# Kernel tuning notes

Hardware: AMD Instinct MI355X
Metric: run time of the kernel (lower is better)

The kernel has to match this reference:

```python
import jax, jax.numpy as jnp
import numpy as np

ALPHA = 0.5  # leak/integration rate of the EI cell

B, L, D = 512, 64, 784
N_EXC, N_INH, N_CLS = 128, 32, 10


def setup_inputs() -> dict:
    key = jax.random.key(0)
    ks = jax.random.split(key, 11)
    s_in = 1.0 / np.sqrt(D)
    s_e = 1.0 / np.sqrt(N_EXC)
    s_i = 1.0 / np.sqrt(N_INH)
    return {
        "x_seq": jax.random.normal(ks[0], (B, L, D), jnp.float32),
        "Wxe": jax.random.normal(ks[1], (N_EXC, D), jnp.float32) * s_in,
        "Wxi": jax.random.normal(ks[2], (N_INH, D), jnp.float32) * s_in,
        "Wee": jax.random.normal(ks[3], (N_EXC, N_EXC), jnp.float32) * s_e,
        "Wie": jax.random.normal(ks[4], (N_EXC, N_INH), jnp.float32) * s_i,
        "Wei": jax.random.normal(ks[5], (N_INH, N_EXC), jnp.float32) * s_e,
        "Wii": jax.random.normal(ks[6], (N_INH, N_INH), jnp.float32) * s_i,
        "be": jax.random.normal(ks[7], (N_EXC,), jnp.float32) * 0.01,
        "bi": jax.random.normal(ks[8], (N_INH,), jnp.float32) * 0.01,
        "W_ro": jax.random.normal(ks[9], (N_CLS, N_EXC), jnp.float32) * s_e,
        "b_ro": jax.random.normal(ks[10], (N_CLS,), jnp.float32) * 0.01,
    }


def reference(x_seq, Wxe, Wxi, Wee, Wie, Wei, Wii, be, bi, W_ro, b_ro):
    # Dale's law: rectify weight magnitudes so exc/inh signs are structural.
    Wxe_p, Wxi_p = jax.nn.relu(Wxe), jax.nn.relu(Wxi)
    Wee_p, Wie_p = jax.nn.relu(Wee), jax.nn.relu(Wie)
    Wei_p, Wii_p = jax.nn.relu(Wei), jax.nn.relu(Wii)

    def step(carry, x_t):  # x_t: [B, D]
        e, i = carry
        r_e = jax.nn.relu(e)
        r_i = jax.nn.relu(i)
        exc_e = x_t @ Wxe_p.T + r_e @ Wee_p.T          # [B, n_exc]
        inh_e = r_i @ Wie_p.T                           # [B, n_exc]
        exc_i = x_t @ Wxi_p.T + r_e @ Wei_p.T           # [B, n_inh]
        inh_i = r_i @ Wii_p.T                           # [B, n_inh]
        e_new = (1.0 - ALPHA) * e + ALPHA * (exc_e - inh_e + be)
        i_new = (1.0 - ALPHA) * i + ALPHA * (exc_i - inh_i + bi)
        r_e_new = jax.nn.relu(e_new)
        r_i_new = jax.nn.relu(i_new)
        bal_e = exc_e - inh_e
        bal_i = exc_i - inh_i
        logits_t = r_e_new @ W_ro.T + b_ro              # readout(F.relu(e))
        return (e_new, i_new), (logits_t, r_e_new, r_i_new, bal_e, bal_i)

    Bn = x_seq.shape[0]
    e0 = jnp.zeros((Bn, Wee.shape[0]), x_seq.dtype)
    i0 = jnp.zeros((Bn, Wii.shape[0]), x_seq.dtype)
    _, outs = jax.lax.scan(step, (e0, i0), jnp.swapaxes(x_seq, 0, 1))  # time-major
    logits_seq, r_e_seq, r_i_seq, bal_e_seq, bal_i_seq = (
        jnp.swapaxes(o, 0, 1) for o in outs)  # back to [B, L, ...]
    return logits_seq, logits_seq[:, -1, :], r_e_seq, r_i_seq, bal_e_seq, bal_i_seq
```

## Files before the change

### kernel.cpp

```cpp
#include <hip/hip_runtime.h>

#define NE 128
#define NI 32
#define NT 160
#define NC 10
#define BB 512
#define LL 64
#define DD 784
#define KP 800
#define MM (BB*LL)

#define G_OFF   0
#define G_SZ    (NT*NT)
#define WH_OFF  (G_OFF + G_SZ)
#define WL_OFF  (WH_OFF + 64000)
#define U_OFF   (WL_OFF + 64000)
#define U_SZ    (MM*NT)

#define O_LOGITS 0
#define O_LAST   327680
#define O_RE     332800
#define O_RI     4527104
#define O_BALE   5575680
#define O_BALI   9769984

#define LDS_BARRIER() asm volatile("s_waitcnt lgkmcnt(0)\n\ts_barrier" ::: "memory")

typedef __attribute__((ext_vector_type(8))) short short8;
typedef __attribute__((ext_vector_type(4))) float af4;

static __device__ __forceinline__ unsigned short f2bf(float f) {
  unsigned u = __float_as_uint(f);
  return (unsigned short)((u + 0x7FFFu + ((u >> 16) & 1u)) >> 16);
}
static __device__ __forceinline__ float bf2f(unsigned short h) {
  return __uint_as_float((unsigned)h << 16);
}

__global__ void prep_kernel(const float* __restrict__ Wxe, const float* __restrict__ Wxi,
                            const float* __restrict__ Wee, const float* __restrict__ Wie,
                            const float* __restrict__ Wei, const float* __restrict__ Wii,
                            float* __restrict__ ws) {
  int idx = blockIdx.x * blockDim.x + threadIdx.x;
  const int total = G_SZ + NT * KP;
  if (idx >= total) return;
  if (idx < G_SZ) {
    int k = idx / NT, j = idx % NT;
    float g;
    if (j < NE) {
      if (k < NE) g =  fmaxf(Wee[j*NE + k], 0.f);
      else        g = -fmaxf(Wie[j*NI + (k-NE)], 0.f);
    } else {
      int ji = j - NE;
      if (k < NE) g =  fmaxf(Wei[ji*NE + k], 0.f);
      else        g = -fmaxf(Wii[ji*NI + (k-NE)], 0.f);
    }
    ws[G_OFF + k*NT + j] = g;
  } else {
    int t = idx - G_SZ;
    int n = t / KP, k = t - n * KP;
    float v = 0.f;
    if (k < DD)
      v = (n < NE) ? fmaxf(Wxe[n*DD + k], 0.f) : fmaxf(Wxi[(n-NE)*DD + k], 0.f);
    unsigned short h = f2bf(v);
    unsigned short l = f2bf(v - bf2f(h));
    ((unsigned short*)(ws + WH_OFF))[t] = h;
    ((unsigned short*)(ws + WL_OFF))[t] = l;
  }
}

__global__ __launch_bounds__(256, 1) void gemm_kernel(const float* __restrict__ X,
                                                      const float* __restrict__ ws,
                                                      float* __restrict__ U) {
  const int tid  = threadIdx.x;
  const int lane = tid & 63;
  const int wave = tid >> 6;
  const int n16  = lane & 15;
  const int quad = lane >> 4;
  const int mbase = blockIdx.x * 128 + wave * 32;

  const unsigned short* Wh = (const unsigned short*)(ws + WH_OFF);
  const unsigned short* Wl = (const unsigned short*)(ws + WL_OFF);

  af4 acc[2][10];
  #pragma unroll
  for (int ms = 0; ms < 2; ++ms)
    #pragma unroll
    for (int nt = 0; nt < 10; ++nt)
      #pragma unroll
      for (int r = 0; r < 4; ++r) acc[ms][nt][r] = 0.f;

  const float* xrow[2] = { X + (size_t)(mbase + n16) * DD,
                           X + (size_t)(mbase + 16 + n16) * DD };

  for (int ks = 0; ks < 24; ++ks) {
    const int kb = ks * 32 + quad * 8;
    short8 ah[2], al[2];
    #pragma unroll
    for (int ms = 0; ms < 2; ++ms) {
      float4 v0 = *(const float4*)(xrow[ms] + kb);
      float4 v1 = *(const float4*)(xrow[ms] + kb + 4);
      float f[8] = {v0.x, v0.y, v0.z, v0.w, v1.x, v1.y, v1.z, v1.w};
      #pragma unroll
      for (int j = 0; j < 8; ++j) {
        unsigned short h = f2bf(f[j]);
        ah[ms][j] = (short)h;
        al[ms][j] = (short)f2bf(f[j] - bf2f(h));
      }
    }
    short8 bh[10], bl[10];
    #pragma unroll
    for (int nt = 0; nt < 10; ++nt) {
      const size_t off = (size_t)(nt * 16 + n16) * KP + kb;
      bh[nt] = *(const short8*)(Wh + off);
      bl[nt] = *(const short8*)(Wl + off);
    }
    #pragma unroll
    for (int ms = 0; ms < 2; ++ms)
      #pragma unroll
      for (int nt = 0; nt < 10; ++nt) {
        acc[ms][nt] = __builtin_amdgcn_mfma_f32_16x16x32_bf16(ah[ms], bh[nt], acc[ms][nt], 0, 0, 0);
        acc[ms][nt] = __builtin_amdgcn_mfma_f32_16x16x32_bf16(ah[ms], bl[nt], acc[ms][nt], 0, 0, 0);
        acc[ms][nt] = __builtin_amdgcn_mfma_f32_16x16x32_bf16(al[ms], bh[nt], acc[ms][nt], 0, 0, 0);
      }
  }

  {
    const int kb = 768 + quad * 8;
    const bool ok = kb < DD;
    short8 ah[2], al[2];
    #pragma unroll
    for (int ms = 0; ms < 2; ++ms) {
      float f[8] = {0,0,0,0,0,0,0,0};
      if (ok) {
        float4 v0 = *(const float4*)(xrow[ms] + kb);
        float4 v1 = *(const float4*)(xrow[ms] + kb + 4);
        f[0]=v0.x; f[1]=v0.y; f[2]=v0.z; f[3]=v0.w;
        f[4]=v1.x; f[5]=v1.y; f[6]=v1.z; f[7]=v1.w;
      }
      #pragma unroll
      for (int j = 0; j < 8; ++j) {
        unsigned short h = f2bf(f[j]);
        ah[ms][j] = (short)h;
        al[ms][j] = (short)f2bf(f[j] - bf2f(h));
      }
    }
    short8 bh[10], bl[10];
    #pragma unroll
    for (int nt = 0; nt < 10; ++nt) {
      const size_t off = (size_t)(nt * 16 + n16) * KP + kb;
      bh[nt] = *(const short8*)(Wh + off);
      bl[nt] = *(const short8*)(Wl + off);
    }
    #pragma unroll
    for (int ms = 0; ms < 2; ++ms)
      #pragma unroll
      for (int nt = 0; nt < 10; ++nt) {
        acc[ms][nt] = __builtin_amdgcn_mfma_f32_16x16x32_bf16(ah[ms], bh[nt], acc[ms][nt], 0, 0, 0);
        acc[ms][nt] = __builtin_amdgcn_mfma_f32_16x16x32_bf16(ah[ms], bl[nt], acc[ms][nt], 0, 0, 0);
        acc[ms][nt] = __builtin_amdgcn_mfma_f32_16x16x32_bf16(al[ms], bh[nt], acc[ms][nt], 0, 0, 0);
      }
  }

  #pragma unroll
  for (int ms = 0; ms < 2; ++ms)
    #pragma unroll
    for (int nt = 0; nt < 10; ++nt)
      #pragma unroll
      for (int r = 0; r < 4; ++r) {
        const int row = mbase + ms * 16 + quad * 4 + r;
        U[(size_t)row * NT + nt * 16 + n16] = acc[ms][nt][r];
      }
}

__global__ __launch_bounds__(256, 2) void recur_kernel(
    const float* __restrict__ ws,
    const float* __restrict__ be, const float* __restrict__ bi,
    float* __restrict__ out) {
  __shared__ float rbuf[2][NT];
  __shared__ float balbuf[2][NT];
  __shared__ float biasL[NT];

  const int tid  = threadIdx.x;
  const int lane = tid & 63;
  const int wave = tid >> 6;
  const int jc   = (wave << 3) | (lane & 7);
  const int kc   = (lane >> 3) & 7;
  const int j0   = jc * 5;
  const int k0   = kc * 20;
  const int b    = blockIdx.x;

  const float* G = ws + G_OFF;
  const float* U = ws + U_OFF;

  float g[20][5];
  #pragma unroll
  for (int kk = 0; kk < 20; ++kk)
    #pragma unroll
    for (int c = 0; c < 5; ++c)
      g[kk][c] = G[(size_t)(k0 + kk) * NT + j0 + c];

  if (tid < NT) biasL[tid] = (tid < NE) ? be[tid] : bi[tid - NE];
  for (int i = tid; i < 2 * NT; i += 256) (&rbuf[0][0])[i] = 0.f;

  const bool owner = (kc == 0);
  float u[5];
  if (owner) {
    const size_t ub = ((size_t)b * LL) * NT + j0;
    #pragma unroll
    for (int c = 0; c < 5; ++c) u[c] = U[ub + c];
  }
  float s[5];
  #pragma unroll
  for (int c = 0; c < 5; ++c) s[c] = 0.f;

  __syncthreads();

  for (int l = 0; l < LL; ++l) {
    const int p = l & 1;
    if (l > 0) {
      const size_t ob = (size_t)b * LL + (l - 1);
      if (tid < NE) {
        out[O_RE   + ob * NE + tid] = rbuf[p][tid];
        out[O_BALE + ob * NE + tid] = balbuf[p][tid];
      } else if (tid < NT) {
        const int j2 = tid - NE;
        out[O_RI   + ob * NI + j2] = rbuf[p][NE + j2];
        out[O_BALI + ob * NI + j2] = balbuf[p][NE + j2];
      }
    }
    float nu[5];
    if (owner && l + 1 < LL) {
      const size_t nb = ((size_t)b * LL + (l + 1)) * NT + j0;
      #pragma unroll
      for (int c = 0; c < 5; ++c) nu[c] = U[nb + c];
    }
    float a[5];
    #pragma unroll
    for (int c = 0; c < 5; ++c) a[c] = 0.f;
    #pragma unroll
    for (int kk4 = 0; kk4 < 5; ++kk4) {
      float4 rv = *(const float4*)(&rbuf[p][k0 + kk4 * 4]);
      #pragma unroll
      for (int c = 0; c < 5; ++c)
        a[c] += rv.x * g[kk4*4+0][c] + rv.y * g[kk4*4+1][c]
              + rv.z * g[kk4*4+2][c] + rv.w * g[kk4*4+3][c];
    }
    #pragma unroll
    for (int c = 0; c < 5; ++c) {
      float v = a[c];
      v += __shfl_xor(v, 8, 64);
      v += __shfl_xor(v, 16, 64);
      v += __shfl_xor(v, 32, 64);
      a[c] = v;
    }
    if (owner) {
      #pragma unroll
      for (int c = 0; c < 5; ++c) {
        float bal = a[c] + u[c];
        balbuf[1 - p][j0 + c] = bal;
        float sn = 0.5f * (s[c] + bal + biasL[j0 + c]);
        s[c] = sn;
        rbuf[1 - p][j0 + c] = fmaxf(sn, 0.f);
      }
      #pragma unroll
      for (int c = 0; c < 5; ++c) u[c] = nu[c];
    }
    LDS_BARRIER();
  }
  {
    const size_t ob = (size_t)b * LL + 63;
    if (tid < NE) {
      out[O_RE   + ob * NE + tid] = rbuf[0][tid];
      out[O_BALE + ob * NE + tid] = balbuf[0][tid];
    } else if (tid < NT) {
      const int j2 = tid - NE;
      out[O_RI   + ob * NI + j2] = rbuf[0][NE + j2];
      out[O_BALI + ob * NI + j2] = balbuf[0][NE + j2];
    }
  }
}

__global__ __launch_bounds__(256) void logits_kernel(const float* __restrict__ Wro,
                                                     const float* __restrict__ bro,
                                                     float* __restrict__ out) {
  __shared__ float WroL[NC * 132];
  __shared__ float broL[NC];
  const int tid = threadIdx.x;
  for (int i = tid; i < NC * NE; i += 256) {
    int c = i >> 7, k = i & 127;
    WroL[c * 132 + k] = Wro[i];
  }
  if (tid < NC) broL[tid] = bro[tid];
  __syncthreads();
  const int idx = blockIdx.x * 256 + tid;
  const int m = idx / 10, c = idx - m * 10;
  const float* re = out + O_RE + (size_t)m * NE;
  float v = broL[c];
  #pragma unroll
  for (int t4 = 0; t4 < 32; ++t4) {
    float4 rv = *(const float4*)(re + t4 * 4);
    float4 wv = *(const float4*)(&WroL[c * 132 + t4 * 4]);
    v += rv.x * wv.x + rv.y * wv.y + rv.z * wv.z + rv.w * wv.w;
  }
  out[O_LOGITS + (size_t)m * NC + c] = v;
  if ((m & 63) == 63) out[O_LAST + (size_t)(m >> 6) * NC + c] = v;
}

extern "C" void kernel_launch(void* const* d_in, const int* in_sizes, int n_in,
                              void* d_out, int out_size, void* d_ws, size_t ws_size,
                              hipStream_t stream) {
  const float* x   = (const float*)d_in[0];
  const float* Wxe = (const float*)d_in[1];
  const float* Wxi = (const float*)d_in[2];
  const float* Wee = (const float*)d_in[3];
  const float* Wie = (const float*)d_in[4];
  const float* Wei = (const float*)d_in[5];
  const float* Wii = (const float*)d_in[6];
  const float* be  = (const float*)d_in[7];
  const float* bi  = (const float*)d_in[8];
  const float* Wro = (const float*)d_in[9];
  const float* bro = (const float*)d_in[10];
  float* ws  = (float*)d_ws;
  float* out = (float*)d_out;

  hipLaunchKernelGGL(prep_kernel, dim3((G_SZ + NT*KP + 255)/256), dim3(256), 0, stream,
                     Wxe, Wxi, Wee, Wie, Wei, Wii, ws);
  hipLaunchKernelGGL(gemm_kernel, dim3(MM/128), dim3(256), 0, stream,
                     x, ws, ws + U_OFF);
  hipLaunchKernelGGL(recur_kernel, dim3(BB), dim3(256), 0, stream,
                     ws, be, bi, out);
  hipLaunchKernelGGL(logits_kernel, dim3(MM * NC / 256), dim3(256), 0, stream,
                     Wro, bro, out);
}
```

Baseline: 314.3 us.

## Shrink GEMM tile per wave, prefetch X, use packed bf16 split conversion

```diff
diff --git a/kernel.cpp b/kernel.cpp
--- a/kernel.cpp
+++ b/kernel.cpp
@@ -35,6 +35,22 @@
 }
 static __device__ __forceinline__ float bf2f(unsigned short h) {
   return __uint_as_float((unsigned)h << 16);
+}
+
+static __device__ __forceinline__ void cvt_split8(const float* f, short8& ah, short8& al) {
+  union { short8 s; unsigned u[4]; } H, L;
+  #pragma unroll
+  for (int p = 0; p < 4; ++p) {
+    float lo = f[2*p], hi = f[2*p+1];
+    unsigned h;
+    asm("v_cvt_pk_bf16_f32 %0, %1, %2" : "=v"(h) : "v"(lo), "v"(hi));
+    float rl = lo - __uint_as_float(h << 16);
+    float rh = hi - __uint_as_float(h & 0xffff0000u);
+    unsigned l;
+    asm("v_cvt_pk_bf16_f32 %0, %1, %2" : "=v"(l) : "v"(rl), "v"(rh));
+    H.u[p] = h; L.u[p] = l;
+  }
+  ah = H.s; al = L.s;
 }
 
 __global__ void prep_kernel(const float* __restrict__ Wxe, const float* __restrict__ Wxi,
@@ -69,7 +85,7 @@
   }
 }
 
-__global__ __launch_bounds__(256, 1) void gemm_kernel(const float* __restrict__ X,
+__global__ __launch_bounds__(256, 2) void gemm_kernel(const float* __restrict__ X,
                                                       const float* __restrict__ ws,
                                                       float* __restrict__ U) {
   const int tid  = threadIdx.x;
@@ -77,35 +93,38 @@
   const int wave = tid >> 6;
   const int n16  = lane & 15;
   const int quad = lane >> 4;
-  const int mbase = blockIdx.x * 128 + wave * 32;
+  const int mbase = blockIdx.x * 64 + wave * 16;
 
   const unsigned short* Wh = (const unsigned short*)(ws + WH_OFF);
   const unsigned short* Wl = (const unsigned short*)(ws + WL_OFF);
 
-  af4 acc[2][10];
-  #pragma unroll
-  for (int ms = 0; ms < 2; ++ms)
-    #pragma unroll
-    for (int nt = 0; nt < 10; ++nt)
-      #pragma unroll
-      for (int r = 0; r < 4; ++r) acc[ms][nt][r] = 0.f;
-
-  const float* xrow[2] = { X + (size_t)(mbase + n16) * DD,
-                           X + (size_t)(mbase + 16 + n16) * DD };
+  af4 acc[10];
+  #pragma unroll
+  for (int nt = 0; nt < 10; ++nt)
+    #pragma unroll
+    for (int r = 0; r < 4; ++r) acc[nt][r] = 0.f;
+
+  const float* xrow = X + (size_t)(mbase + n16) * DD;
+
+  float fa[8];
+  {
+    const int kb = quad * 8;
+    float4 v0 = *(const float4*)(xrow + kb);
+    float4 v1 = *(const float4*)(xrow + kb + 4);
+    fa[0]=v0.x; fa[1]=v0.y; fa[2]=v0.z; fa[3]=v0.w;
+    fa[4]=v1.x; fa[5]=v1.y; fa[6]=v1.z; fa[7]=v1.w;
+  }
 
   for (int ks = 0; ks < 24; ++ks) {
     const int kb = ks * 32 + quad * 8;
-    short8 ah[2], al[2];
-    #pragma unroll
-    for (int ms = 0; ms < 2; ++ms) {
-      float4 v0 = *(const float4*)(xrow[ms] + kb);
-      float4 v1 = *(const float4*)(xrow[ms] + kb + 4);
-      float f[8] = {v0.x, v0.y, v0.z, v0.w, v1.x, v1.y, v1.z, v1.w};
-      #pragma unroll
-      for (int j = 0; j < 8; ++j) {
-        unsigned short h = f2bf(f[j]);
-        ah[ms][j] = (short)h;
-        al[ms][j] = (short)f2bf(f[j] - bf2f(h));
+    float nf[8] = {0,0,0,0,0,0,0,0};
+    {
+      const int nkb = kb + 32;
+      if (nkb < DD) {
+        float4 v0 = *(const float4*)(xrow + nkb);
+        float4 v1 = *(const float4*)(xrow + nkb + 4);
+        nf[0]=v0.x; nf[1]=v0.y; nf[2]=v0.z; nf[3]=v0.w;
+        nf[4]=v1.x; nf[5]=v1.y; nf[6]=v1.z; nf[7]=v1.w;
       }
     }
     short8 bh[10], bl[10];
@@ -115,36 +134,20 @@
       bh[nt] = *(const short8*)(Wh + off);
       bl[nt] = *(const short8*)(Wl + off);
     }
-    #pragma unroll
-    for (int ms = 0; ms < 2; ++ms)
-      #pragma unroll
-      for (int nt = 0; nt < 10; ++nt) {
-        acc[ms][nt] = __builtin_amdgcn_mfma_f32_16x16x32_bf16(ah[ms], bh[nt], acc[ms][nt], 0, 0, 0);
-        acc[ms][nt] = __builtin_amdgcn_mfma_f32_16x16x32_bf16(ah[ms], bl[nt], acc[ms][nt], 0, 0, 0);
-        acc[ms][nt] = __builtin_amdgcn_mfma_f32_16x16x32_bf16(al[ms], bh[nt], acc[ms][nt], 0, 0, 0);
-      }
+    short8 ah, al;
+    cvt_split8(fa, ah, al);
+    #pragma unroll
+    for (int nt = 0; nt < 10; ++nt) {
+      acc[nt] = __builtin_amdgcn_mfma_f32_16x16x32_bf16(ah, bh[nt], acc[nt], 0, 0, 0);
+      acc[nt] = __builtin_amdgcn_mfma_f32_16x16x32_bf16(ah, bl[nt], acc[nt], 0, 0, 0);
+      acc[nt] = __builtin_amdgcn_mfma_f32_16x16x32_bf16(al, bh[nt], acc[nt], 0, 0, 0);
+    }
+    #pragma unroll
+    for (int j = 0; j < 8; ++j) fa[j] = nf[j];
   }
 
   {
     const int kb = 768 + quad * 8;
-    const bool ok = kb < DD;
-    short8 ah[2], al[2];
-    #pragma unroll
-    for (int ms = 0; ms < 2; ++ms) {
-      float f[8] = {0,0,0,0,0,0,0,0};
-      if (ok) {
-        float4 v0 = *(const float4*)(xrow[ms] + kb);
-        float4 v1 = *(const float4*)(xrow[ms] + kb + 4);
-        f[0]=v0.x; f[1]=v0.y; f[2]=v0.z; f[3]=v0.w;
-        f[4]=v1.x; f[5]=v1.y; f[6]=v1.z; f[7]=v1.w;
-      }
-      #pragma unroll
-      for (int j = 0; j < 8; ++j) {
-        unsigned short h = f2bf(f[j]);
-        ah[ms][j] = (short)h;
-        al[ms][j] = (short)f2bf(f[j] - bf2f(h));
-      }
-    }
     short8 bh[10], bl[10];
     #pragma unroll
     for (int nt = 0; nt < 10; ++nt) {
@@ -152,25 +155,23 @@
       bh[nt] = *(const short8*)(Wh + off);
       bl[nt] = *(const short8*)(Wl + off);
     }
-    #pragma unroll
-    for (int ms = 0; ms < 2; ++ms)
-      #pragma unroll
-      for (int nt = 0; nt < 10; ++nt) {
-        acc[ms][nt] = __builtin_amdgcn_mfma_f32_16x16x32_bf16(ah[ms], bh[nt], acc[ms][nt], 0, 0, 0);
-        acc[ms][nt] = __builtin_amdgcn_mfma_f32_16x16x32_bf16(ah[ms], bl[nt], acc[ms][nt], 0, 0, 0);
-        acc[ms][nt] = __builtin_amdgcn_mfma_f32_16x16x32_bf16(al[ms], bh[nt], acc[ms][nt], 0, 0, 0);
-      }
-  }
-
-  #pragma unroll
-  for (int ms = 0; ms < 2; ++ms)
-    #pragma unroll
-    for (int nt = 0; nt < 10; ++nt)
-      #pragma unroll
-      for (int r = 0; r < 4; ++r) {
-        const int row = mbase + ms * 16 + quad * 4 + r;
-        U[(size_t)row * NT + nt * 16 + n16] = acc[ms][nt][r];
-      }
+    short8 ah, al;
+    cvt_split8(fa, ah, al);
+    #pragma unroll
+    for (int nt = 0; nt < 10; ++nt) {
+      acc[nt] = __builtin_amdgcn_mfma_f32_16x16x32_bf16(ah, bh[nt], acc[nt], 0, 0, 0);
+      acc[nt] = __builtin_amdgcn_mfma_f32_16x16x32_bf16(ah, bl[nt], acc[nt], 0, 0, 0);
+      acc[nt] = __builtin_amdgcn_mfma_f32_16x16x32_bf16(al, bh[nt], acc[nt], 0, 0, 0);
+    }
+  }
+
+  #pragma unroll
+  for (int nt = 0; nt < 10; ++nt)
+    #pragma unroll
+    for (int r = 0; r < 4; ++r) {
+      const int row = mbase + quad * 4 + r;
+      U[(size_t)row * NT + nt * 16 + n16] = acc[nt][r];
+    }
 }
 
 __global__ __launch_bounds__(256, 2) void recur_kernel(
@@ -326,7 +327,7 @@
 
   hipLaunchKernelGGL(prep_kernel, dim3((G_SZ + NT*KP + 255)/256), dim3(256), 0, stream,
                      Wxe, Wxi, Wee, Wie, Wei, Wii, ws);
-  hipLaunchKernelGGL(gemm_kernel, dim3(MM/128), dim3(256), 0, stream,
+  hipLaunchKernelGGL(gemm_kernel, dim3(MM/64), dim3(256), 0, stream,
                      x, ws, ws + U_OFF);
   hipLaunchKernelGGL(recur_kernel, dim3(BB), dim3(256), 0, stream,
                      ws, be, bi, out);
```

Measured after the change: 319.2 us. No clear change (+1.5%).
